# Kernel tuning notes

Measured on AMD Instinct MI355X. Metric: run time of the kernel, lower is better.

Reference implementation:

```python
import jax, jax.numpy as jnp
import numpy as np

B, LS, LW, LV, M, D, H = 256, 1024, 1024, 1024, 16, 5120, 2048

def setup_inputs() -> dict:
    key = jax.random.key(0)
    ks = jax.random.split(key, 8)
    return {
        'phi_batch': jax.random.normal(ks[0], (B, LS), jnp.float32),
        'w_M_real': jax.random.normal(ks[1], (B, LW, M), jnp.float32),
        'w_M_imag': jax.random.normal(ks[2], (B, LW, M), jnp.float32),
        'v_M': jax.random.normal(ks[3], (LV, M), jnp.float32),
        'W1e': jax.random.normal(ks[4], (D, H), jnp.float32) * 0.02,
        'b1e': jnp.zeros((H,), jnp.float32),
        'W2e': jax.random.normal(ks[5], (H, LS), jnp.float32) * 0.02,
        'b2e': jnp.zeros((LS,), jnp.float32),
        'W1r': jax.random.normal(ks[6], (D, H), jnp.float32) * 0.02,
        'b1r': jnp.zeros((H,), jnp.float32),
        'W2r': jax.random.normal(ks[7], (H, 1), jnp.float32) * 0.02,
        'b2r': jnp.zeros((1,), jnp.float32),
    }

def reference(phi_batch, w_M_real, w_M_imag, v_M, W1e, b1e, W2e, b2e, W1r, b1r, W2r, b2r):
    b, ls = phi_batch.shape
    m = v_M.shape[1]
    # s = (1/sqrt(Ls)) * exp(1j*phi); use real/imag parts directly
    mag = 1.0 / jnp.sqrt(jnp.asarray(ls, jnp.float32))
    s_feat = jnp.concatenate([mag * jnp.cos(phi_batch), mag * jnp.sin(phi_batch)], axis=-1)  # [B, 2Ls]
    # Batched concat across (batch, M): replaces the nested Python loops
    X = jnp.concatenate([
        jnp.broadcast_to(s_feat[:, None, :], (b, m, s_feat.shape[-1])),
        jnp.swapaxes(w_M_real, 1, 2),                       # [B, M, Lw]
        jnp.swapaxes(w_M_imag, 1, 2),                       # [B, M, Lw]
        jnp.broadcast_to(v_M.T[None, :, :], (b, m, v_M.shape[0])),
    ], axis=-1)                                             # [B, M, D]
    eta_M = jax.nn.relu(X @ W1e + b1e) @ W2e + b2e          # [B, M, Ls]
    rho_M = (jax.nn.relu(X @ W1r + b1r) @ W2r + b2r)[..., 0]  # [B, M]
    eta = jnp.einsum('bm,bml->bl', rho_M, eta_M)            # sum_m rho_m * eta_m
    phi_optimal = phi_batch - eta
    return phi_optimal, jnp.swapaxes(eta_M, 1, 2)           # [B, Ls], [B, Ls, M]
```

## Files before the change

kernel.cpp:

```cpp
#include <hip/hip_runtime.h>
#include <hip/hip_bf16.h>
#include <stdint.h>

#define B_    256
#define LS_   1024
#define LW_   1024
#define LV_   1024
#define M_    16
#define D_    5120
#define H_    2048
#define ROWS  4096
#define N1    4096
#define KW    2048

typedef __hip_bfloat16 bf16;
typedef __bf16 bf16x8 __attribute__((ext_vector_type(8)));
typedef __bf16 bf16x4 __attribute__((ext_vector_type(4)));
typedef float f32x4 __attribute__((ext_vector_type(4)));

#define SB0() __builtin_amdgcn_sched_barrier(0)
#define LGKM(n) asm volatile("s_waitcnt lgkmcnt(" #n ")" ::: "memory")
#define VMC(n)  asm volatile("s_waitcnt vmcnt(" #n ")" ::: "memory")

__device__ __forceinline__ void gld_lds16(const void* g, void* l) {
  auto gp = (const __attribute__((address_space(1))) uint32_t*)(uintptr_t)g;
  auto lp = (__attribute__((address_space(3))) uint32_t*)(uint32_t)(uintptr_t)l;
  __builtin_amdgcn_global_load_lds(gp, lp, 16, 0, 0);
}

__device__ __forceinline__ void transpose64_body(char* sm, const float* __restrict__ in,
                                                 bf16* __restrict__ out,
                                                 int C, int R, int r0, int c0, int t) {
  float (*tile)[65] = (float (*)[65])sm;
  const int tx = t & 15, ty = t >> 4;
#pragma unroll
  for (int i = 0; i < 4; ++i) {
    const float4 v = *(const float4*)&in[(size_t)(r0 + ty + i * 16) * C + c0 + tx * 4];
    tile[ty + i * 16][tx * 4 + 0] = v.x;
    tile[ty + i * 16][tx * 4 + 1] = v.y;
    tile[ty + i * 16][tx * 4 + 2] = v.z;
    tile[ty + i * 16][tx * 4 + 3] = v.w;
  }
  __syncthreads();
#pragma unroll
  for (int i = 0; i < 4; ++i) {
    const int n = c0 + ty + i * 16;
    bf16x4 o;
#pragma unroll
    for (int j = 0; j < 4; ++j) o[j] = (__bf16)tile[tx * 4 + j][ty + i * 16];
    *(bf16x4*)&out[(size_t)n * R + r0 + tx * 4] = o;
  }
}

__global__ void __launch_bounds__(256)
prep_kernel(const float* __restrict__ phi,
            const float* __restrict__ wMr, const float* __restrict__ wMi,
            const float* __restrict__ vM,
            const float* __restrict__ W1e, const float* __restrict__ W1r,
            const float* __restrict__ W2e,
            bf16* __restrict__ sfeat, bf16* __restrict__ Awr,
            bf16* __restrict__ W1sT, bf16* __restrict__ W1wT,
            bf16* __restrict__ W2t, float* __restrict__ hVT) {
  __shared__ __align__(16) char sm[32768];
  const int bid = blockIdx.x;
  const int t = threadIdx.x;

  if (bid < 256) {
    float (*vs)[16] = (float (*)[16])sm;
    float (*ws)[16] = (float (*)[16])(sm + 16384);
    const float* Wb = (bid < 128) ? W1e : W1r;
    const int nbase = (bid & 127) * 16;
    const int nout = ((bid < 128) ? 0 : 2048) + nbase;
    const int m = t & 15, nl = t >> 4;
    float acc = 0.f;
    for (int l0 = 0; l0 < 1024; l0 += 256) {
      __syncthreads();
#pragma unroll
      for (int i = 0; i < 16; ++i) {
        int e = i * 256 + t, l = e >> 4, n = e & 15;
        vs[l][n] = vM[(size_t)(l0 + l) * 16 + n];
        ws[l][n] = Wb[(size_t)(4096 + l0 + l) * 2048 + nbase + n];
      }
      __syncthreads();
#pragma unroll 8
      for (int ll = 0; ll < 256; ++ll)
        acc += vs[ll][m] * ws[ll][nl];
    }
    hVT[(size_t)(nout + nl) * 16 + m] = acc;
  } else if (bid < 4352) {
    const int idx = bid - 256;
    const int z = idx >> 10, rem = idx & 1023;
    const float* src = (z == 0 || z == 2) ? W1e : W1r;
    src += (z < 2) ? 0 : (size_t)2048 * 2048;
    bf16* dst = (z < 2) ? W1sT : W1wT;
    dst += (z == 0 || z == 2) ? 0 : (size_t)2048 * 2048;
    transpose64_body(sm, src, dst, 2048, 2048, (rem >> 5) * 64, (rem & 31) * 64, t);
  } else if (bid < 4864) {
    const int idx = bid - 4352;
    transpose64_body(sm, W2e, W2t, LS_, H_, (idx >> 4) * 64, (idx & 15) * 64, t);
  } else if (bid < 8960) {
    const int idx = bid - 4864;
    const int b = idx >> 4, l0 = (idx & 15) * 64;
    float (*tr)[17] = (float (*)[17])sm;
    float (*ti)[17] = (float (*)[17])(sm + 4352 * 4);
    const float* wrb = wMr + (size_t)b * (LW_ * M_) + (size_t)l0 * 16;
    const float* wib = wMi + (size_t)b * (LW_ * M_) + (size_t)l0 * 16;
#pragma unroll
    for (int i = 0; i < 4; ++i) {
      int e = i * 256 + t, l = e >> 4, m = e & 15;
      tr[l][m] = wrb[e];
      ti[l][m] = wib[e];
    }
    __syncthreads();
    int m = t >> 4, t4 = t & 15;
    bf16* outR = Awr + (size_t)(b * 16 + m) * KW + l0;
#pragma unroll
    for (int j = 0; j < 4; ++j) outR[t4 * 4 + j]        = __float2bfloat16(tr[t4 * 4 + j][m]);
#pragma unroll
    for (int j = 0; j < 4; ++j) outR[1024 + t4 * 4 + j] = __float2bfloat16(ti[t4 * 4 + j][m]);
  } else {
    const int i = (bid - 8960) * 256 + t;
    const int b = i >> 10, l = i & 1023;
    float p = phi[i];
    float s, c;
    sincosf(p, &s, &c);
    sfeat[b * 2048 + l]        = __float2bfloat16(0.03125f * c);
    sfeat[b * 2048 + 1024 + l] = __float2bfloat16(0.03125f * s);
  }
}

__global__ void __launch_bounds__(256)
hsum_kernel(const float* __restrict__ hSp, const float* __restrict__ b1e,
            const float* __restrict__ b1r, float* __restrict__ hS2) {
  const int i = (blockIdx.x * 256 + threadIdx.x) * 4;
  const int c = i & (N1 - 1);
  f32x4 v = *(const f32x4*)&hSp[i];
  v = v + *(const f32x4*)&hSp[(size_t)B_ * N1 + i];
  v = v + *(const f32x4*)&hSp[(size_t)2 * B_ * N1 + i];
  v = v + *(const f32x4*)&hSp[(size_t)3 * B_ * N1 + i];
  const float* bp = (c < H_) ? &b1e[c] : &b1r[c - H_];
  v = v + *(const f32x4*)bp;
  *(f32x4*)&hS2[i] = v;
}

__global__ void __launch_bounds__(512, 2)
gemm1_256_kernel(const bf16* __restrict__ A, const bf16* __restrict__ Bt,
                 const float* __restrict__ hS2, const float* __restrict__ hVT,
                 const float* __restrict__ w2r,
                 bf16* __restrict__ outH, float* __restrict__ rhoP) {
  extern __shared__ __align__(16) char smem[];
  constexpr int NT = KW / 32;

  const int tid  = threadIdx.x;
  const int lane = tid & 63;
  const int wave = tid >> 6;
  const int wr = wave >> 2, wc = wave & 3;
  const int fr = lane & 15, fq = lane >> 4;
  const int row0 = blockIdx.y * 256, col0 = blockIdx.x * 256;

  const int slotF = (((fr & 1) << 2) | fq) ^ ((fr >> 1) & 7);
  const int aOff = (wr << 13) + ((fr >> 1) << 7) + (slotF << 4);
  const int bOff = 16384 + (wc << 12) + ((fr >> 1) << 7) + (slotF << 4);

  const int lg0 = (tid >> 3), lg1 = 64 + (tid >> 3);
  const int su0 = (tid & 7) ^ (lg0 & 7), su1 = (tid & 7) ^ (lg1 & 7);
  const int rowp0 = lg0 * 2 + (su0 >> 2), rowp1 = lg1 * 2 + (su1 >> 2);
  const int kb0 = (su0 & 3) << 4, kb1 = (su1 & 3) << 4;
  const char* pA0 = (const char*)A  + (size_t)(row0 + rowp0) * (KW * 2) + kb0;
  const char* pA1 = (const char*)A  + (size_t)(row0 + rowp1) * (KW * 2) + kb1;
  const char* pB0 = (const char*)Bt + (size_t)(col0 + rowp0) * (KW * 2) + kb0;
  const char* pB1 = (const char*)Bt + (size_t)(col0 + rowp1) * (KW * 2) + kb1;

  auto stageTile = [&](int T) {
    char* dst = smem + (size_t)(T & 3) * 32768;
    const size_t ko = (size_t)T * 64;
    gld_lds16(pA0 + ko, dst + 0     + tid * 16);
    gld_lds16(pA1 + ko, dst + 8192  + tid * 16);
    gld_lds16(pB0 + ko, dst + 16384 + tid * 16);
    gld_lds16(pB1 + ko, dst + 24576 + tid * 16);
  };

  f32x4 acc[8][4] = {};
  bf16x8 a[8];
  bf16x8 bA[4], bB[4];

  stageTile(0); stageTile(1); stageTile(2);
  VMC(4);
  __builtin_amdgcn_s_barrier();
  {
    const char* aP0 = smem + aOff;
    const char* bP0 = smem + bOff;
#pragma unroll
    for (int m = 0; m < 4; ++m) a[m] = *(const bf16x8*)(aP0 + m * 1024);
#pragma unroll
    for (int n = 0; n < 4; ++n) bA[n] = *(const bf16x8*)(bP0 + n * 1024);
  }
  SB0();

  auto doIter = [&](int T, bf16x8 (&bCur)[4], bf16x8 (&bNxt)[4]) {
    const char* aP  = smem + (size_t)(T & 3) * 32768 + aOff;
    const char* aPn = smem + (size_t)((T + 1) & 3) * 32768 + aOff;
    const char* bPn = smem + (size_t)((T + 1) & 3) * 32768 + bOff;
    const bool rb = (T + 1 < NT);
    const bool pf = (T + 3 < NT);

    LGKM(0);
    SB0();
#pragma unroll
    for (int m = 4; m < 8; ++m) a[m] = *(const bf16x8*)(aP + m * 1024);
    SB0();
    __builtin_amdgcn_s_setprio(1);
#pragma unroll
    for (int m = 0; m < 4; ++m)
#pragma unroll
      for (int n = 0; n < 4; ++n)
        acc[m][n] = __builtin_amdgcn_mfma_f32_16x16x32_bf16(a[m], bCur[n], acc[m][n], 0, 0, 0);
    __builtin_amdgcn_s_setprio(0);
    SB0();

    if (pf) stageTile(T + 3);
    LGKM(0);
    SB0();
    if (rb) {
#pragma unroll
      for (int m = 0; m < 4; ++m) a[m] = *(const bf16x8*)(aPn + m * 1024);
#pragma unroll
      for (int n = 0; n < 4; ++n) bNxt[n] = *(const bf16x8*)(bPn + n * 1024);
    }
    SB0();
    __builtin_amdgcn_s_setprio(1);
#pragma unroll
    for (int m = 4; m < 8; ++m)
#pragma unroll
      for (int n = 0; n < 4; ++n)
        acc[m][n] = __builtin_amdgcn_mfma_f32_16x16x32_bf16(a[m], bCur[n], acc[m][n], 0, 0, 0);
    __builtin_amdgcn_s_setprio(0);
    SB0();
    if (pf) { VMC(4); }
    else    { VMC(0); }
    __builtin_amdgcn_s_barrier();
  };

  for (int t = 0; t < NT; t += 2) {
    doIter(t,     bA, bB);
    doIter(t + 1, bB, bA);
  }

  if (col0 < H_) {
#pragma unroll
    for (int n = 0; n < 4; ++n) {
      const int c = col0 + wc * 64 + n * 16 + fr;
      const f32x4 hv = *(const f32x4*)&hVT[(size_t)c * 16 + fq * 4];
#pragma unroll
      for (int m = 0; m < 8; ++m) {
        const int rbase = row0 + wr * 128 + m * 16;
        const float hs = hS2[(size_t)(rbase >> 4) * N1 + c];
#pragma unroll
        for (int j = 0; j < 4; ++j) {
          const int r = rbase + fq * 4 + j;
          float v = acc[m][n][j] + hs + hv[j];
          outH[(size_t)r * N1 + c] = __float2bfloat16(v > 0.f ? v : 0.f);
        }
      }
    }
  } else {
    const int cb = (col0 >> 8) - 8;
    float* rhoT = (float*)smem;
    f32x4 hv4[4];
    float w2[4];
#pragma unroll
    for (int n = 0; n < 4; ++n) {
      const int c = col0 + wc * 64 + n * 16 + fr;
      hv4[n] = *(const f32x4*)&hVT[(size_t)c * 16 + fq * 4];
      w2[n] = w2r[c - H_];
    }
#pragma unroll
    for (int m = 0; m < 8; ++m) {
      const int rbase = row0 + wr * 128 + m * 16;
      const float* hrow = &hS2[(size_t)(rbase >> 4) * N1];
      f32x4 rsv = {0.f, 0.f, 0.f, 0.f};
#pragma unroll
      for (int n = 0; n < 4; ++n) {
        const int c = col0 + wc * 64 + n * 16 + fr;
        const float hs = hrow[c];
#pragma unroll
        for (int j = 0; j < 4; ++j) {
          float v = acc[m][n][j] + hs + hv4[n][j];
          v = v > 0.f ? v : 0.f;
          rsv[j] += v * w2[n];
        }
      }
#pragma unroll
      for (int j = 0; j < 4; ++j) {
        rsv[j] += __shfl_xor(rsv[j], 1);
        rsv[j] += __shfl_xor(rsv[j], 2);
        rsv[j] += __shfl_xor(rsv[j], 4);
        rsv[j] += __shfl_xor(rsv[j], 8);
      }
      if (fr == 0)
        *(f32x4*)&rhoT[((wr * 4 + wc) << 7) + m * 16 + fq * 4] = rsv;
    }
    __syncthreads();
    if (tid < 256) {
      const int wrr = tid >> 7, lr = tid & 127;
      const float* rt = &rhoT[(wrr * 4) << 7];
      const float s = rt[lr] + rt[128 + lr] + rt[256 + lr] + rt[384 + lr];
      rhoP[(size_t)(row0 + wrr * 128 + lr) * 8 + cb] = s;
    }
  }
}

template <int EPI, int NT>
__global__ void __launch_bounds__(256, 2)
gemm128_pipe_kernel(const bf16* __restrict__ A, int lda,
                    const bf16* __restrict__ Bt, int ldb,
                    const float* __restrict__ bias0,
                    const float* __restrict__ rhoP, const float* __restrict__ b2r,
                    const float* __restrict__ phi,
                    float* __restrict__ outS, float* __restrict__ out0) {
  extern __shared__ __align__(16) char smem[];

  if (EPI == 1) {
    const int z = blockIdx.z;
    A    += (size_t)z * 512;
    Bt   += (size_t)z * 512;
    outS += (size_t)z * ((size_t)B_ * N1);
  }

  const int tid  = threadIdx.x;
  const int lane = tid & 63;
  const int wave = tid >> 6;
  const int wr = wave >> 1, wc = wave & 1;
  const int fr = lane & 15, fq = lane >> 4;
  const int row0 = blockIdx.y * 128, col0 = blockIdx.x * 128;

  if (EPI == 0) {
    if (tid < 128) {
      const float* pp = &rhoP[(size_t)(row0 + tid) * 8];
      const f32x4 p0 = *(const f32x4*)pp;
      const f32x4 p1 = *(const f32x4*)(pp + 4);
      const float s = p0[0] + p0[1] + p0[2] + p0[3] +
                      p1[0] + p1[1] + p1[2] + p1[3] + b2r[0];
      ((float*)(smem + 65536))[tid] = s;
    }
    LGKM(0);
    SB0();
  }

  const int slotF = (((fr & 1) << 2) | fq) ^ ((fr >> 1) & 7);
  const int aOff = (wr << 12) + ((fr >> 1) << 7) + (slotF << 4);
  const int bOff = 8192 + (wc << 12) + ((fr >> 1) << 7) + (slotF << 4);

  const int lgl = tid >> 3;
  const int su  = (tid & 7) ^ (lgl & 7);
  const int rp0 = lgl * 2 + (su >> 2);
  const int rp1 = (32 + lgl) * 2 + (su >> 2);
  const int kb  = (su & 3) << 4;
  const char* pA0 = (const char*)A  + (size_t)(row0 + rp0) * ((size_t)lda * 2) + kb;
  const char* pA1 = (const char*)A  + (size_t)(row0 + rp1) * ((size_t)lda * 2) + kb;
  const char* pB0 = (const char*)Bt + (size_t)(col0 + rp0) * ((size_t)ldb * 2) + kb;
  const char* pB1 = (const char*)Bt + (size_t)(col0 + rp1) * ((size_t)ldb * 2) + kb;

  auto stageTile = [&](int T) {
    char* dst = smem + (size_t)(T & 3) * 16384;
    const size_t ko = (size_t)T * 64;
    gld_lds16(pA0 + ko, dst + 0     + tid * 16);
    gld_lds16(pA1 + ko, dst + 4096  + tid * 16);
    gld_lds16(pB0 + ko, dst + 8192  + tid * 16);
    gld_lds16(pB1 + ko, dst + 12288 + tid * 16);
  };

  f32x4 acc[4][4] = {};
  bf16x8 aA[4], aB[4], bA[4], bB[4];

  stageTile(0); stageTile(1); stageTile(2);
  VMC(4);
  __builtin_amdgcn_s_barrier();
  {
    const char* aP0 = smem + aOff;
    const char* bP0 = smem + bOff;
#pragma unroll
    for (int m = 0; m < 4; ++m) aA[m] = *(const bf16x8*)(aP0 + m * 1024);
#pragma unroll
    for (int n = 0; n < 4; ++n) bA[n] = *(const bf16x8*)(bP0 + n * 1024);
  }
  SB0();

  auto doIter = [&](int T, bf16x8 (&aCur)[4], bf16x8 (&bCur)[4],
                    bf16x8 (&aNxt)[4], bf16x8 (&bNxt)[4]) {
    const char* aPn = smem + (size_t)((T + 1) & 3) * 16384 + aOff;
    const char* bPn = smem + (size_t)((T + 1) & 3) * 16384 + bOff;
    const bool rb = (T + 1 < NT);
    const bool pf = (T + 3 < NT);

    if (pf) stageTile(T + 3);
    LGKM(0);
    SB0();
    if (rb) {
#pragma unroll
      for (int m = 0; m < 4; ++m) aNxt[m] = *(const bf16x8*)(aPn + m * 1024);
#pragma unroll
      for (int n = 0; n < 4; ++n) bNxt[n] = *(const bf16x8*)(bPn + n * 1024);
    }
    SB0();
    __builtin_amdgcn_s_setprio(1);
#pragma unroll
    for (int m = 0; m < 4; ++m)
#pragma unroll
      for (int n = 0; n < 4; ++n)
        acc[m][n] = __builtin_amdgcn_mfma_f32_16x16x32_bf16(aCur[m], bCur[n], acc[m][n], 0, 0, 0);
    __builtin_amdgcn_s_setprio(0);
    SB0();
    if (pf) { VMC(4); }
    else    { VMC(0); }
    __builtin_amdgcn_s_barrier();
  };

  for (int t = 0; t < NT; t += 2) {
    doIter(t,     aA, bA, aB, bB);
    doIter(t + 1, aB, bB, aA, bA);
  }

  if (EPI == 0) {
    const float* rhoL = (const float*)(smem + 65536);
#pragma unroll
    for (int m = 0; m < 4; ++m) {
      const int bg = (row0 >> 4) + wr * 4 + m;
      const f32x4 rv = *(const f32x4*)&rhoL[wr * 64 + m * 16 + fq * 4];
#pragma unroll
      for (int n = 0; n < 4; ++n) {
        const int c = col0 + wc * 64 + n * 16 + fr;
        const float bias = bias0[c];
        float part = 0.f;
#pragma unroll
        for (int j = 0; j < 4; ++j) {
          float v = acc[m][n][j] + bias;
          outS[(size_t)bg * (LS_ * M_) + (size_t)c * M_ + (fq * 4 + j)] = v;
          part += rv[j] * v;
        }
        part += __shfl_xor(part, 16);
        part += __shfl_xor(part, 32);
        if (fq == 0)
          out0[(size_t)bg * LS_ + c] = phi[(size_t)bg * LS_ + c] - part;
      }
    }
  } else {
#pragma unroll
    for (int m = 0; m < 4; ++m) {
#pragma unroll
      for (int n = 0; n < 4; ++n) {
        const int c = col0 + wc * 64 + n * 16 + fr;
#pragma unroll
        for (int j = 0; j < 4; ++j) {
          const int r = row0 + wr * 64 + m * 16 + fq * 4 + j;
          outS[(size_t)r * N1 + c] = acc[m][n][j];
        }
      }
    }
  }
}

extern "C" void kernel_launch(void* const* d_in, const int* in_sizes, int n_in,
                              void* d_out, int out_size, void* d_ws, size_t ws_size,
                              hipStream_t stream) {
  const float* phi = (const float*)d_in[0];
  const float* wMr = (const float*)d_in[1];
  const float* wMi = (const float*)d_in[2];
  const float* vM  = (const float*)d_in[3];
  const float* W1e = (const float*)d_in[4];
  const float* b1e = (const float*)d_in[5];
  const float* W2e = (const float*)d_in[6];
  const float* b2e = (const float*)d_in[7];
  const float* W1r = (const float*)d_in[8];
  const float* b1r = (const float*)d_in[9];
  const float* W2r = (const float*)d_in[10];
  const float* b2r = (const float*)d_in[11];

  float* out0 = (float*)d_out;
  float* out1 = out0 + (size_t)B_ * LS_;

  bf16* Awr   = (bf16*)d_ws;
  bf16* W1sT  = Awr  + (size_t)ROWS * KW;
  bf16* W1wT  = W1sT + (size_t)N1 * KW;
  bf16* h     = W1wT + (size_t)N1 * KW;
  bf16* W2t   = h + (size_t)ROWS * N1;
  bf16* sfeat = W2t + (size_t)LS_ * H_;
  float* hSp  = (float*)(sfeat + (size_t)B_ * 2048);
  float* hS2  = hSp + (size_t)4 * B_ * N1;
  float* hVT  = hS2 + (size_t)B_ * N1;
  float* rhoP = hVT + (size_t)N1 * 16;

  (void)hipFuncSetAttribute(reinterpret_cast<const void*>(gemm1_256_kernel),
                            hipFuncAttributeMaxDynamicSharedMemorySize, 131072);
  (void)hipFuncSetAttribute(reinterpret_cast<const void*>(gemm128_pipe_kernel<0, 64>),
                            hipFuncAttributeMaxDynamicSharedMemorySize, 66048);
  (void)hipFuncSetAttribute(reinterpret_cast<const void*>(gemm128_pipe_kernel<1, 16>),
                            hipFuncAttributeMaxDynamicSharedMemorySize, 65536);

  prep_kernel<<<9984, 256, 0, stream>>>(phi, wMr, wMi, vM, W1e, W1r, W2e,
                                        sfeat, Awr, W1sT, W1wT, W2t, hVT);

  gemm128_pipe_kernel<1, 16><<<dim3(N1 / 128, B_ / 128, 4), 256, 65536, stream>>>(
      sfeat, 2048, W1sT, KW, nullptr, nullptr, nullptr, nullptr, hSp, nullptr);

  hsum_kernel<<<(B_ * N1 / 4) / 256, 256, 0, stream>>>(hSp, b1e, b1r, hS2);

  gemm1_256_kernel<<<dim3(N1 / 256, ROWS / 256), 512, 131072, stream>>>(
      Awr, W1wT, hS2, hVT, W2r, h, rhoP);

  gemm128_pipe_kernel<0, 64><<<dim3(LS_ / 128, ROWS / 128), 256, 66048, stream>>>(
      h, N1, W2t, H_, b2e, rhoP, b2r, phi, out1, out0);
}
```

Measured before the change: 144.3 us.

## Restructure GEMM1 main loop into 64-wide K tiles with eight-phase double buffering

Result: faster. 141.0 us (-2.3%).

```diff
diff --git a/kernel.cpp b/kernel.cpp
--- a/kernel.cpp
+++ b/kernel.cpp
@@ -21,6 +21,7 @@
 #define SB0() __builtin_amdgcn_sched_barrier(0)
 #define LGKM(n) asm volatile("s_waitcnt lgkmcnt(" #n ")" ::: "memory")
 #define VMC(n)  asm volatile("s_waitcnt vmcnt(" #n ")" ::: "memory")
+#define BARv()  __builtin_amdgcn_s_barrier()
 
 __device__ __forceinline__ void gld_lds16(const void* g, void* l) {
   auto gp = (const __attribute__((address_space(1))) uint32_t*)(uintptr_t)g;
@@ -149,7 +150,8 @@
                  const float* __restrict__ w2r,
                  bf16* __restrict__ outH, float* __restrict__ rhoP) {
   extern __shared__ __align__(16) char smem[];
-  constexpr int NT = KW / 32;
+  constexpr int NKT = KW / 64;
+  constexpr int NI  = NKT / 2;
 
   const int tid  = threadIdx.x;
   const int lane = tid & 63;
@@ -158,92 +160,114 @@
   const int fr = lane & 15, fq = lane >> 4;
   const int row0 = blockIdx.y * 256, col0 = blockIdx.x * 256;
 
-  const int slotF = (((fr & 1) << 2) | fq) ^ ((fr >> 1) & 7);
-  const int aOff = (wr << 13) + ((fr >> 1) << 7) + (slotF << 4);
-  const int bOff = 16384 + (wc << 12) + ((fr >> 1) << 7) + (slotF << 4);
-
-  const int lg0 = (tid >> 3), lg1 = 64 + (tid >> 3);
-  const int su0 = (tid & 7) ^ (lg0 & 7), su1 = (tid & 7) ^ (lg1 & 7);
-  const int rowp0 = lg0 * 2 + (su0 >> 2), rowp1 = lg1 * 2 + (su1 >> 2);
-  const int kb0 = (su0 & 3) << 4, kb1 = (su1 & 3) << 4;
-  const char* pA0 = (const char*)A  + (size_t)(row0 + rowp0) * (KW * 2) + kb0;
-  const char* pA1 = (const char*)A  + (size_t)(row0 + rowp1) * (KW * 2) + kb1;
-  const char* pB0 = (const char*)Bt + (size_t)(col0 + rowp0) * (KW * 2) + kb0;
-  const char* pB1 = (const char*)Bt + (size_t)(col0 + rowp1) * (KW * 2) + kb1;
-
-  auto stageTile = [&](int T) {
-    char* dst = smem + (size_t)(T & 3) * 32768;
-    const size_t ko = (size_t)T * 64;
-    gld_lds16(pA0 + ko, dst + 0     + tid * 16);
-    gld_lds16(pA1 + ko, dst + 8192  + tid * 16);
-    gld_lds16(pB0 + ko, dst + 16384 + tid * 16);
-    gld_lds16(pB1 + ko, dst + 24576 + tid * 16);
+  const int xr  = fr & 7;
+  const int sK0 = ((fq ^ xr) << 4);
+  const int sK1 = (((4 + fq) ^ xr) << 4);
+  const int aRowB = (wr * 128 + fr) << 7;
+  const int bRowB = 32768 + ((wc * 64 + fr) << 7);
+
+  const char* gA = (const char*)A  + (size_t)row0 * (KW * 2);
+  const char* gB = (const char*)Bt + (size_t)col0 * (KW * 2);
+  char* buf0 = smem;
+  char* buf1 = smem + 65536;
+
+  const int srow  = tid >> 3;
+  const int slotU = (tid & 7) ^ (srow & 7);
+
+  auto stageHalf = [&](const char* g, char* ldsOp, int half, int kt) {
+#pragma unroll
+    for (int r = 0; r < 2; ++r) {
+      const int row = half * 128 + r * 64 + srow;
+      gld_lds16(g + (size_t)row * (KW * 2) + (size_t)kt * 128 + slotU * 16,
+                ldsOp + half * 16384 + r * 8192 + tid * 16);
+    }
   };
 
   f32x4 acc[8][4] = {};
-  bf16x8 a[8];
-  bf16x8 bA[4], bB[4];
-
-  stageTile(0); stageTile(1); stageTile(2);
-  VMC(4);
-  __builtin_amdgcn_s_barrier();
-  {
-    const char* aP0 = smem + aOff;
-    const char* bP0 = smem + bOff;
-#pragma unroll
-    for (int m = 0; m < 4; ++m) a[m] = *(const bf16x8*)(aP0 + m * 1024);
-#pragma unroll
-    for (int n = 0; n < 4; ++n) bA[n] = *(const bf16x8*)(bP0 + n * 1024);
-  }
-  SB0();
-
-  auto doIter = [&](int T, bf16x8 (&bCur)[4], bf16x8 (&bNxt)[4]) {
-    const char* aP  = smem + (size_t)(T & 3) * 32768 + aOff;
-    const char* aPn = smem + (size_t)((T + 1) & 3) * 32768 + aOff;
-    const char* bPn = smem + (size_t)((T + 1) & 3) * 32768 + bOff;
-    const bool rb = (T + 1 < NT);
-    const bool pf = (T + 3 < NT);
-
-    LGKM(0);
-    SB0();
-#pragma unroll
-    for (int m = 4; m < 8; ++m) a[m] = *(const bf16x8*)(aP + m * 1024);
-    SB0();
+
+  auto readA4 = [&](const char* buf, int mg, int sk, bf16x8 (&a)[4]) {
+    const char* p = buf + aRowB + mg * 8192 + sk;
+#pragma unroll
+    for (int i = 0; i < 4; ++i) a[i] = *(const bf16x8*)(p + i * 2048);
+  };
+  auto readB4 = [&](const char* buf, int sk, bf16x8 (&b)[4]) {
+    const char* p = buf + bRowB + sk;
+#pragma unroll
+    for (int n = 0; n < 4; ++n) b[n] = *(const bf16x8*)(p + n * 2048);
+  };
+  auto mma16 = [&](int mg, bf16x8 (&a)[4], bf16x8 (&b)[4]) {
     __builtin_amdgcn_s_setprio(1);
 #pragma unroll
-    for (int m = 0; m < 4; ++m)
+    for (int i = 0; i < 4; ++i)
 #pragma unroll
       for (int n = 0; n < 4; ++n)
-        acc[m][n] = __builtin_amdgcn_mfma_f32_16x16x32_bf16(a[m], bCur[n], acc[m][n], 0, 0, 0);
+        acc[mg * 4 + i][n] =
+            __builtin_amdgcn_mfma_f32_16x16x32_bf16(a[i], b[n], acc[mg * 4 + i][n], 0, 0, 0);
     __builtin_amdgcn_s_setprio(0);
-    SB0();
-
-    if (pf) stageTile(T + 3);
-    LGKM(0);
-    SB0();
-    if (rb) {
-#pragma unroll
-      for (int m = 0; m < 4; ++m) a[m] = *(const bf16x8*)(aPn + m * 1024);
-#pragma unroll
-      for (int n = 0; n < 4; ++n) bNxt[n] = *(const bf16x8*)(bPn + n * 1024);
-    }
-    SB0();
-    __builtin_amdgcn_s_setprio(1);
-#pragma unroll
-    for (int m = 4; m < 8; ++m)
-#pragma unroll
-      for (int n = 0; n < 4; ++n)
-        acc[m][n] = __builtin_amdgcn_mfma_f32_16x16x32_bf16(a[m], bCur[n], acc[m][n], 0, 0, 0);
-    __builtin_amdgcn_s_setprio(0);
-    SB0();
-    if (pf) { VMC(4); }
+  };
+
+  stageHalf(gB, buf0 + 32768, 0, 0);
+  stageHalf(gB, buf0 + 32768, 1, 0);
+  stageHalf(gA, buf0, 0, 0);
+  stageHalf(gA, buf0, 1, 0);
+  stageHalf(gB, buf1 + 32768, 0, 1);
+  VMC(2);
+  BARv();
+
+  for (int t = 0; t < NI; ++t) {
+    const int k1 = 2 * t + 1;
+    const bool pf = (t + 1 < NI);
+    bf16x8 aX[4], aY[4], b0[4], b1[4];
+
+    readA4(buf0, 0, sK0, aX); readB4(buf0, sK0, b0);
+    stageHalf(gB, buf1 + 32768, 1, k1);
+    BARv(); LGKM(0); SB0();
+    mma16(0, aX, b0);
+    SB0(); BARv();
+
+    readA4(buf0, 1, sK0, aY);
+    stageHalf(gA, buf1, 0, k1);
+    BARv(); LGKM(0); SB0();
+    mma16(1, aY, b0);
+    SB0(); BARv();
+
+    readA4(buf0, 0, sK1, aX); readB4(buf0, sK1, b1);
+    stageHalf(gA, buf1, 1, k1);
+    BARv(); LGKM(0); SB0();
+    mma16(0, aX, b1);
+    SB0(); BARv();
+
+    readA4(buf0, 1, sK1, aY);
+    if (pf) { stageHalf(gB, buf0 + 32768, 0, 2 * t + 2); VMC(2); }
     else    { VMC(0); }
-    __builtin_amdgcn_s_barrier();
-  };
-
-  for (int t = 0; t < NT; t += 2) {
-    doIter(t,     bA, bB);
-    doIter(t + 1, bB, bA);
+    BARv(); LGKM(0); SB0();
+    mma16(1, aY, b1);
+    SB0(); BARv();
+
+    readA4(buf1, 0, sK0, aX); readB4(buf1, sK0, b0);
+    if (pf) stageHalf(gB, buf0 + 32768, 1, 2 * t + 2);
+    BARv(); LGKM(0); SB0();
+    mma16(0, aX, b0);
+    SB0(); BARv();
+
+    readA4(buf1, 1, sK0, aY);
+    if (pf) stageHalf(gA, buf0, 0, 2 * t + 2);
+    BARv(); LGKM(0); SB0();
+    mma16(1, aY, b0);
+    SB0(); BARv();
+
+    readA4(buf1, 0, sK1, aX); readB4(buf1, sK1, b1);
+    if (pf) stageHalf(gA, buf0, 1, 2 * t + 2);
+    BARv(); LGKM(0); SB0();
+    mma16(0, aX, b1);
+    SB0(); BARv();
+
+    readA4(buf1, 1, sK1, aY);
+    if (pf) { stageHalf(gB, buf1 + 32768, 0, 2 * t + 3); VMC(2); }
+    else    { VMC(0); }
+    BARv(); LGKM(0); SB0();
+    mma16(1, aY, b1);
+    SB0(); BARv();
   }
 
   if (col0 < H_) {
```
